# Optimization experiments

Hardware: AMD Instinct MI355X
Metric: run time of the kernel (lower is better)

The kernel has to match this reference:

```python
import jax, jax.numpy as jnp
import numpy as np

TAU = 2.0       # LIF membrane time constant (spikingjelly default)
ALPHA = 2.0     # ATan surrogate sharpness
EPS = 1e-5      # BN eps
NUM_HEADS = 12
PATCH = 2
LENTH = 256     # (H/PATCH)*(W/PATCH)

@jax.custom_vjp
def heaviside(x):
    return (x >= 0.0).astype(x.dtype)

def _hv_fwd(x):
    return heaviside(x), x

def _hv_bwd(x, g):
    sg = ALPHA / 2.0 / (1.0 + (jnp.pi / 2.0 * ALPHA * x) ** 2)  # ATan surrogate
    return (g * sg,)

heaviside.defvjp(_hv_fwd, _hv_bwd)

def lif(x):
    # multi-step LIF over leading time axis, hard reset, v_th = 1.0
    def step(v, xt):
        v = v + (xt - v) / TAU
        s = heaviside(v - 1.0)
        return v * (1.0 - s), s
    _, s = jax.lax.scan(step, jnp.zeros_like(x[0]), x)
    return s

def setup_inputs() -> dict:
    key = jax.random.key(0)
    ks = jax.random.split(key, 9)
    T, B, C, H, W = 4, 4, 384, 32, 32
    x = jax.random.normal(ks[0], (T, B, C, H, W), dtype=jnp.float32)
    Wconv = jax.random.normal(ks[1], (2 * C, C, PATCH, PATCH), dtype=jnp.float32) * (1.0 / np.sqrt(C * PATCH * PATCH))
    gamma1 = jax.random.uniform(ks[2], (2 * C,), dtype=jnp.float32, minval=0.5, maxval=1.5)
    beta1 = jax.random.normal(ks[3], (2 * C,), dtype=jnp.float32) * 0.1
    Wproj = jax.random.normal(ks[4], (C, C), dtype=jnp.float32) * (1.0 / np.sqrt(C))
    gamma2 = jax.random.uniform(ks[5], (C,), dtype=jnp.float32, minval=0.5, maxval=1.5)
    beta2 = jax.random.normal(ks[6], (C,), dtype=jnp.float32) * 0.1
    firing_rate_x = jax.random.uniform(ks[7], (1, 1, NUM_HEADS, 1, 1), dtype=jnp.float32, minval=0.05, maxval=0.5)
    firing_rate_attn = jax.random.uniform(ks[8], (1, 1, NUM_HEADS, 1, 1), dtype=jnp.float32, minval=0.05, maxval=0.5)
    return {"x": x, "Wconv": Wconv, "gamma1": gamma1, "beta1": beta1, "Wproj": Wproj,
            "gamma2": gamma2, "beta2": beta2, "firing_rate_x": firing_rate_x,
            "firing_rate_attn": firing_rate_attn}

def reference(x, Wconv, gamma1, beta1, Wproj, gamma2, beta2, firing_rate_x, firing_rate_attn):
    T, B, C, H, W = x.shape
    d = C // NUM_HEADS
    xs = lif(x)                                          # spikes [T,B,C,H,W]
    # patch conv dim -> 2*dim, stride = kernel = PATCH (eval BN: running mean 0, var 1)
    y = jax.lax.conv_general_dilated(xs.reshape(T * B, C, H, W), Wconv,
                                     (PATCH, PATCH), 'VALID',
                                     dimension_numbers=('NCHW', 'OIHW', 'NCHW'))
    bn1 = gamma1 / jnp.sqrt(1.0 + EPS)
    y = y * bn1[None, :, None, None] + beta1[None, :, None, None]
    Np = (H // PATCH) * (W // PATCH)                     # == LENTH
    y = y.reshape(T, B, NUM_HEADS, 2 * d, Np)
    y1, y2 = y[:, :, :, :d, :], y[:, :, :, d:, :]
    xr = xs.reshape(T, B, NUM_HEADS, d, H * W)
    scale1 = 1.0 / jnp.sqrt(firing_rate_x * d)
    attn = jnp.einsum('tbhdn,tbhdm->tbhnm', y1, xr) * scale1   # [T,B,h,Np,HW]
    attn = lif(attn)
    scale2 = 1.0 / jnp.sqrt(firing_rate_attn * LENTH)
    out = jnp.einsum('tbhdn,tbhnm->tbhdm', y2, attn) * scale2  # [T,B,h,d,HW]
    out = out.reshape(T, B, C, H, W)
    out = lif(out)
    out = jnp.einsum('oc,tbchw->tbohw', Wproj, out)            # 1x1 conv proj
    bn2 = gamma2 / jnp.sqrt(1.0 + EPS)
    out = out * bn2[None, None, :, None, None] + beta2[None, None, :, None, None]
    return out + x
```

## Files before the change

### kernel.cpp

```cpp
#include <hip/hip_runtime.h>
#include <hip/hip_bf16.h>
#include <math.h>


typedef __attribute__((ext_vector_type(8))) short short8;
typedef __attribute__((ext_vector_type(4))) float f32x4;

#define T_ 4
#define B_ 4
#define C_ 384
#define HW 1024
#define NH_ 12
#define Np_ 256
#define EPS_ 1e-5f
#define LDK 56

static __device__ __forceinline__ unsigned short f2bf(float f) {
    __hip_bfloat16 h = __float2bfloat16(f);
    return *reinterpret_cast<unsigned short*>(&h);
}
static __device__ __forceinline__ float bf2f(unsigned short u) {
    __hip_bfloat16 h = *reinterpret_cast<__hip_bfloat16*>(&u);
    return __bfloat162float(h);
}
static __device__ __forceinline__ void split3(float w, unsigned short& u0,
                                              unsigned short& u1, unsigned short& u2) {
    u0 = f2bf(w);  float f0 = bf2f(u0);
    float r1 = w - f0;
    u1 = f2bf(r1); float f1 = bf2f(u1);
    u2 = f2bf(r1 - f1);
}

__global__ __launch_bounds__(256) void k_wsplit(const float* __restrict__ Wc,
                                                const float* __restrict__ Wp,
                                                unsigned short* __restrict__ Wc3,
                                                unsigned short* __restrict__ Wp3) {
    const int NC = 768 * 1536;
    const int NP = 384 * 384;
    int i = blockIdx.x * 256 + threadIdx.x;
    float w; unsigned short* dst; int idx, plane;
    if (i < NC) { w = Wc[i]; dst = Wc3; idx = i; plane = NC; }
    else {
        int j = i - NC;
        if (j >= NP) return;
        w = Wp[j]; dst = Wp3; idx = j; plane = NP;
    }
    unsigned short u0, u1, u2;
    split3(w, u0, u1, u2);
    dst[idx] = u0; dst[plane + idx] = u1; dst[2 * plane + idx] = u2;
}

__global__ __launch_bounds__(256) void k_lif_im2col(const float* __restrict__ x,
                                                    unsigned short* __restrict__ Bc,
                                                    unsigned short* __restrict__ xsb) {
    int gt = blockIdx.x * 256 + threadIdx.x;
    int pw = gt & 15, ph = (gt >> 4) & 15;
    int v = gt >> 8;
    int c = v % 384, b = v / 384;
    float v00 = 0.f, v01 = 0.f, v10 = 0.f, v11 = 0.f;
    const size_t xrow = ((size_t)b * C_ + c) * HW + (size_t)(2 * ph) * 32 + 2 * pw;
#pragma unroll
    for (int t = 0; t < T_; ++t) {
        const float* px = x + (size_t)t * (B_ * C_ * HW) + xrow;
        float2 r0 = *(const float2*)px;
        float2 r1 = *(const float2*)(px + 32);
        v00 += (r0.x - v00) * 0.5f;
        v01 += (r0.y - v01) * 0.5f;
        v10 += (r1.x - v10) * 0.5f;
        v11 += (r1.y - v11) * 0.5f;
        ushort4 s;
        s.x = (v00 >= 1.f) ? 0x3F80 : 0; if (v00 >= 1.f) v00 = 0.f;
        s.y = (v01 >= 1.f) ? 0x3F80 : 0; if (v01 >= 1.f) v01 = 0.f;
        s.z = (v10 >= 1.f) ? 0x3F80 : 0; if (v10 >= 1.f) v10 = 0.f;
        s.w = (v11 >= 1.f) ? 0x3F80 : 0; if (v11 >= 1.f) v11 = 0.f;
        int tb = t * B_ + b;
        int n = tb * 256 + ph * 16 + pw;
        *(ushort4*)(Bc + (size_t)n * 1536 + 4 * c) = s;
        size_t xo = ((size_t)tb * C_ + c) * HW + (size_t)(2 * ph) * 32 + 2 * pw;
        ushort2 w0 = {s.x, s.y}, w1 = {s.z, s.w};
        *(ushort2*)(xsb + xo) = w0;
        *(ushort2*)(xsb + xo + 32) = w1;
    }
}

__global__ __launch_bounds__(256) void k_mconv(const unsigned short* __restrict__ Bc,
                                               const unsigned short* __restrict__ Wc3,
                                               const float* __restrict__ g1,
                                               const float* __restrict__ b1,
                                               const float* __restrict__ frx,
                                               const float* __restrict__ fra,
                                               unsigned short* __restrict__ y1s,
                                               unsigned short* __restrict__ y2s) {
    __shared__ short As[3][48][LDK];
    __shared__ short Bs[128][LDK];
    const int nb = blockIdx.x, mb = blockIdx.y;
    const int tid = threadIdx.x;
    const int lane = tid & 63, wv = tid >> 6;
    const int quad = lane >> 4, lr = lane & 15;
    f32x4 acc[3][2];
#pragma unroll
    for (int mi = 0; mi < 3; ++mi)
#pragma unroll
        for (int in = 0; in < 2; ++in)
            acc[mi][in] = (f32x4){0.f, 0.f, 0.f, 0.f};

    const int arow = tid >> 2, akoff = (tid & 3) * 8;
    for (int k0 = 0; k0 < 1536; k0 += 32) {
        if (tid < 192) {
#pragma unroll
            for (int s = 0; s < 3; ++s) {
                short8 a = *(const short8*)(Wc3 + ((size_t)(s * 768 + mb * 48 + arow)) * 1536 + k0 + akoff);
                *(short8*)&As[s][arow][akoff] = a;
            }
        }
#pragma unroll
        for (int i = 0; i < 2; ++i) {
            int f = i * 256 + tid;
            int row = f >> 2, koff = (f & 3) * 8;
            short8 bv = *(const short8*)(Bc + ((size_t)(nb * 128 + row)) * 1536 + k0 + koff);
            *(short8*)&Bs[row][koff] = bv;
        }
        __syncthreads();
        short8 bf[2], af[3][3];
#pragma unroll
        for (int in = 0; in < 2; ++in)
            bf[in] = *(const short8*)&Bs[wv * 32 + in * 16 + lr][quad * 8];
#pragma unroll
        for (int s = 0; s < 3; ++s)
#pragma unroll
            for (int mi = 0; mi < 3; ++mi)
                af[s][mi] = *(const short8*)&As[s][mi * 16 + lr][quad * 8];
#pragma unroll
        for (int s = 0; s < 3; ++s)
#pragma unroll
            for (int mi = 0; mi < 3; ++mi)
#pragma unroll
                for (int in = 0; in < 2; ++in)
                    acc[mi][in] = __builtin_amdgcn_mfma_f32_16x16x32_bf16(af[s][mi], bf[in], acc[mi][in], 0, 0, 0);
        __syncthreads();
    }
    const float rs = 1.0f / sqrtf(1.0f + EPS_);
#pragma unroll
    for (int mi = 0; mi < 3; ++mi) {
        const int g16 = 3 * mb + mi;
        const int h = g16 >> 2;
        const int rr16 = (g16 & 3) * 16;
        const bool isy1 = (rr16 < 32);
        const float scl = isy1 ? (1.0f / sqrtf(frx[h] * 32.0f))
                               : (1.0f / sqrtf(fra[h] * 256.0f));
#pragma unroll
        for (int in = 0; in < 2; ++in) {
            int n_g = nb * 128 + wv * 32 + in * 16 + lr;
            int tb = n_g >> 8, pn = n_g & 255;
            size_t base = (size_t)(tb * NH_ + h) * 3 * 8192;
            ushort4 o0, o1, o2;
#pragma unroll
            for (int r = 0; r < 4; ++r) {
                int oc = h * 64 + rr16 + quad * 4 + r;
                float val = (acc[mi][in][r] * (g1[oc] * rs) + b1[oc]) * scl;
                unsigned short u0, u1, u2;
                split3(val, u0, u1, u2);
                ((unsigned short*)&o0)[r] = u0;
                ((unsigned short*)&o1)[r] = u1;
                ((unsigned short*)&o2)[r] = u2;
            }
            if (isy1) {
                int dd = rr16 + quad * 4;
                *(ushort4*)&y1s[base + 0 * 8192 + (size_t)pn * 32 + dd] = o0;
                *(ushort4*)&y1s[base + 1 * 8192 + (size_t)pn * 32 + dd] = o1;
                *(ushort4*)&y1s[base + 2 * 8192 + (size_t)pn * 32 + dd] = o2;
            } else {
                int dd = (rr16 - 32) + quad * 4;
#pragma unroll
                for (int r = 0; r < 4; ++r) {
                    y2s[base + 0 * 8192 + (size_t)(dd + r) * 256 + pn] = ((unsigned short*)&o0)[r];
                    y2s[base + 1 * 8192 + (size_t)(dd + r) * 256 + pn] = ((unsigned short*)&o1)[r];
                    y2s[base + 2 * 8192 + (size_t)(dd + r) * 256 + pn] = ((unsigned short*)&o2)[r];
                }
            }
        }
    }
}

__global__ __launch_bounds__(256, 2) void k_attn_qk(const unsigned short* __restrict__ xsb,
                                                    const unsigned short* __restrict__ y1s,
                                                    unsigned short* __restrict__ abq) {
    __shared__ unsigned short xb[4][64][40];
    const int h = blockIdx.y, b = blockIdx.z;
    const int tid = threadIdx.x;
    const int lane = tid & 63, wq = tid >> 6;
    const int quad = lane >> 4, lr = lane & 15;
    const int m0 = blockIdx.x * 64;

#pragma unroll
    for (int i = 0; i < 8; ++i) {
        int e = tid + i * 256;
        int j4 = e & 15, d = (e >> 4) & 31, t = e >> 9;
        ushort4 v = *(const ushort4*)(xsb + ((size_t)((t * B_ + b) * C_) + h * 32 + d) * HW + m0 + j4 * 4);
        xb[t][j4 * 4 + 0][d] = v.x;
        xb[t][j4 * 4 + 1][d] = v.y;
        xb[t][j4 * 4 + 2][d] = v.z;
        xb[t][j4 * 4 + 3][d] = v.w;
    }
    __syncthreads();

    float vat[4][4][4];
#pragma unroll
    for (int mi = 0; mi < 4; ++mi)
#pragma unroll
        for (int itl = 0; itl < 4; ++itl)
#pragma unroll
            for (int r = 0; r < 4; ++r) vat[mi][itl][r] = 0.f;

#pragma unroll
    for (int t = 0; t < T_; ++t) {
        const int tb = t * B_ + b;
        const size_t slab = (size_t)(tb * NH_ + h) * 3 * 8192;

        short8 af[3][4];
        const unsigned short* y1p = y1s + slab + (size_t)(wq * 64 + lr) * 32 + quad * 8;
#pragma unroll
        for (int s = 0; s < 3; ++s)
#pragma unroll
            for (int itl = 0; itl < 4; ++itl)
                af[s][itl] = *(const short8*)(y1p + s * 8192 + itl * 512);

#pragma unroll
        for (int mi = 0; mi < 4; ++mi) {
            short8 bx = *(const short8*)&xb[t][mi * 16 + lr][quad * 8];
            f32x4 acc[4];
#pragma unroll
            for (int itl = 0; itl < 4; ++itl) acc[itl] = (f32x4){0.f, 0.f, 0.f, 0.f};
#pragma unroll
            for (int s = 0; s < 3; ++s)
#pragma unroll
                for (int itl = 0; itl < 4; ++itl)
                    acc[itl] = __builtin_amdgcn_mfma_f32_16x16x32_bf16(af[s][itl], bx, acc[itl], 0, 0, 0);

            unsigned int q = 0;
#pragma unroll
            for (int itl = 0; itl < 4; ++itl)
#pragma unroll
                for (int r = 0; r < 4; ++r) {
                    float v = vat[mi][itl][r];
                    v += (acc[itl][r] - v) * 0.5f;
                    bool s = (v >= 1.0f);
                    vat[mi][itl][r] = s ? 0.f : v;
                    q |= (s ? 1u : 0u) << (itl * 4 + r);
                }
            int m = m0 + mi * 16 + lr;
            abq[(((size_t)(tb * NH_ + h) * 1024 + m) * 4 + quad) * 4 + wq] = (unsigned short)q;
        }
    }
}

__global__ __launch_bounds__(256, 1) void k_attn_pv(const unsigned long long* __restrict__ abits,
                                                    const unsigned short* __restrict__ y2s,
                                                    unsigned short* __restrict__ obt) {
    const int h = blockIdx.y, b = blockIdx.z;
    const int tid = threadIdx.x;
    const int lane = tid & 63, wv = tid >> 6;
    const int quad = lane >> 4, lr = lane & 15;
    const int dt = wv >> 1, mg = wv & 1;
    const int mbase = blockIdx.x * 64 + mg * 32;
    const int obase = (quad & 2) << 1;

    float vo[2][4];
#pragma unroll
    for (int mi = 0; mi < 2; ++mi)
#pragma unroll
        for (int r = 0; r < 4; ++r) vo[mi][r] = 0.f;

#pragma unroll
    for (int t = 0; t < T_; ++t) {
        const int tb = t * B_ + b;
        const size_t slab = (size_t)(tb * NH_ + h) * 3 * 8192;

        short8 ay[3][8];
        const unsigned short* y2p = y2s + slab + (size_t)(dt * 16 + lr) * 256 + quad * 8;
#pragma unroll
        for (int s = 0; s < 3; ++s)
#pragma unroll
            for (int kt = 0; kt < 8; ++kt)
                ay[s][kt] = *(const short8*)(y2p + s * 8192 + kt * 32);

#pragma unroll
        for (int mi = 0; mi < 2; ++mi) {
            const int m = mbase + mi * 16 + lr;
            const unsigned long long* ap = abits + ((size_t)(tb * NH_ + h) * 1024 + m) * 4 + (quad & 1) * 2;
            unsigned long long Qa = ap[0];
            unsigned long long Qb = ap[1];

            short8 bs[8];
#pragma unroll
            for (int kt = 0; kt < 8; ++kt) {
                int o = kt * 8 + obase;
                unsigned int a4 = (unsigned int)(Qa >> o) & 15u;
                unsigned int b4 = (unsigned int)(Qb >> o) & 15u;
                union { short8 v; unsigned int w[4]; } u;
                u.w[0] = ((a4 & 1u) ? 0x3F80u : 0u) | ((a4 & 2u) ? 0x3F800000u : 0u);
                u.w[1] = ((a4 & 4u) ? 0x3F80u : 0u) | ((a4 & 8u) ? 0x3F800000u : 0u);
                u.w[2] = ((b4 & 1u) ? 0x3F80u : 0u) | ((b4 & 2u) ? 0x3F800000u : 0u);
                u.w[3] = ((b4 & 4u) ? 0x3F80u : 0u) | ((b4 & 8u) ? 0x3F800000u : 0u);
                bs[kt] = u.v;
            }

            f32x4 acc2 = (f32x4){0.f, 0.f, 0.f, 0.f};
#pragma unroll
            for (int s = 0; s < 3; ++s)
#pragma unroll
                for (int kt = 0; kt < 8; ++kt)
                    acc2 = __builtin_amdgcn_mfma_f32_16x16x32_bf16(ay[s][kt], bs[kt], acc2, 0, 0, 0);

            ushort4 ob;
#pragma unroll
            for (int r = 0; r < 4; ++r) {
                float v = vo[mi][r];
                v += (acc2[r] - v) * 0.5f;
                bool s = (v >= 1.0f);
                ((unsigned short*)&ob)[r] = s ? 0x3F80 : 0;
                vo[mi][r] = s ? 0.f : v;
            }
            *(ushort4*)(obt + ((size_t)tb * HW + m) * C_ + h * 32 + dt * 16 + quad * 4) = ob;
        }
    }
}

__global__ __launch_bounds__(256) void k_mproj(const unsigned short* __restrict__ obt,
                                               const unsigned short* __restrict__ Wp3,
                                               const float* __restrict__ g2,
                                               const float* __restrict__ b2,
                                               const float* __restrict__ x,
                                               float* __restrict__ out) {
    __shared__ short As[3][64][LDK];
    __shared__ short Bs[128][LDK];
    const int nb = blockIdx.x, mb = blockIdx.y;
    const int tid = threadIdx.x;
    const int lane = tid & 63, wave = tid >> 6;
    const int wm = wave >> 1, wn = wave & 1;
    const int quad = lane >> 4, lr = lane & 15;
    const int arow = tid >> 2, akoff = (tid & 3) * 8;
    f32x4 acc[2][4];
#pragma unroll
    for (int im = 0; im < 2; ++im)
#pragma unroll
        for (int in = 0; in < 4; ++in)
            acc[im][in] = (f32x4){0.f, 0.f, 0.f, 0.f};

    for (int k0 = 0; k0 < 384; k0 += 32) {
#pragma unroll
        for (int s = 0; s < 3; ++s) {
            short8 a = *(const short8*)(Wp3 + ((size_t)(s * 384 + mb * 64 + arow)) * 384 + k0 + akoff);
            *(short8*)&As[s][arow][akoff] = a;
        }
#pragma unroll
        for (int i = 0; i < 2; ++i) {
            int f = i * 256 + tid;
            int row = f >> 2, koff = (f & 3) * 8;
            short8 bv = *(const short8*)(obt + ((size_t)(nb * 128 + row)) * 384 + k0 + koff);
            *(short8*)&Bs[row][koff] = bv;
        }
        __syncthreads();
        short8 bf[4], af[3][2];
#pragma unroll
        for (int in = 0; in < 4; ++in)
            bf[in] = *(const short8*)&Bs[wn * 64 + in * 16 + lr][quad * 8];
#pragma unroll
        for (int s = 0; s < 3; ++s)
#pragma unroll
            for (int im = 0; im < 2; ++im)
                af[s][im] = *(const short8*)&As[s][wm * 32 + im * 16 + lr][quad * 8];
#pragma unroll
        for (int s = 0; s < 3; ++s)
#pragma unroll
            for (int im = 0; im < 2; ++im)
#pragma unroll
                for (int in = 0; in < 4; ++in)
                    acc[im][in] = __builtin_amdgcn_mfma_f32_16x16x32_bf16(af[s][im], bf[in], acc[im][in], 0, 0, 0);
        __syncthreads();
    }
    const float rs = 1.0f / sqrtf(1.0f + EPS_);
#pragma unroll
    for (int im = 0; im < 2; ++im) {
#pragma unroll
        for (int in = 0; in < 4; ++in) {
            int n_g = nb * 128 + wn * 64 + in * 16 + lr;
            int tb = n_g >> 10, hw = n_g & 1023;
#pragma unroll
            for (int r = 0; r < 4; ++r) {
                int o = mb * 64 + wm * 32 + im * 16 + quad * 4 + r;
                size_t idx = ((size_t)tb * C_ + o) * HW + hw;
                out[idx] = acc[im][in][r] * (g2[o] * rs) + b2[o] + x[idx];
            }
        }
    }
}

extern "C" void kernel_launch(void* const* d_in, const int* in_sizes, int n_in,
                              void* d_out, int out_size, void* d_ws, size_t ws_size,
                              hipStream_t stream) {
    const float* x      = (const float*)d_in[0];
    const float* Wconv  = (const float*)d_in[1];
    const float* gamma1 = (const float*)d_in[2];
    const float* beta1  = (const float*)d_in[3];
    const float* Wproj  = (const float*)d_in[4];
    const float* gamma2 = (const float*)d_in[5];
    const float* beta2  = (const float*)d_in[6];
    const float* frx    = (const float*)d_in[7];
    const float* fra    = (const float*)d_in[8];
    float* out = (float*)d_out;

    unsigned short* ws16 = (unsigned short*)d_ws;
    unsigned short* Bc  = ws16;
    unsigned short* obt = ws16;
    unsigned short* Wc3 = ws16 + 6291456;
    unsigned short* Wp3 = ws16 + 9830400;
    unsigned short* xsb = ws16 + 10272768;
    unsigned short* y1s = ws16 + 16564224;
    unsigned short* y2s = ws16 + 21282816;
    unsigned long long* abits = (unsigned long long*)(ws16 + 26001408);

    k_wsplit<<<5184, 256, 0, stream>>>(Wconv, Wproj, Wc3, Wp3);
    k_lif_im2col<<<1536, 256, 0, stream>>>(x, Bc, xsb);
    k_mconv<<<dim3(32, 16), 256, 0, stream>>>(Bc, Wc3, gamma1, beta1, frx, fra, y1s, y2s);
    k_attn_qk<<<dim3(16, 12, 4), 256, 0, stream>>>(xsb, y1s, (unsigned short*)abits);
    k_attn_pv<<<dim3(16, 12, 4), 256, 0, stream>>>(abits, y2s, obt);
    k_mproj<<<dim3(128, 6), 256, 0, stream>>>(obt, Wp3, gamma2, beta2, x, out);
}
```

Before: 253.8 us.

## Use direct global-to-LDS loads in conv GEMM and shrink M tile to 32

The patch-conv GEMM now stages its A (3-way bf16 split weights) and B (im2col spikes) tiles with global_load_lds 16-byte direct-to-LDS transfers, which skip the register round trip. The LDS layout becomes unpadded 32-wide rows to match that instruction's contiguous per-wave write pattern. The M tile drops from 48 to 32 rows and the grid grows from 16 to 24 M-blocks, giving more blocks and fewer accumulators per thread. The unpadded LDS rows may cause bank conflicts on the fragment reads, and the loop still uses a single buffer with two barriers per k step.

New measurement: 254.5 us. About the same (+0.3%).

```diff
diff --git a/kernel.cpp b/kernel.cpp
--- a/kernel.cpp
+++ b/kernel.cpp
@@ -29,6 +29,12 @@
     float r1 = w - f0;
     u1 = f2bf(r1); float f1 = bf2f(u1);
     u2 = f2bf(r1 - f1);
+}
+
+typedef const __attribute__((address_space(1))) unsigned int* gas_t;
+typedef __attribute__((address_space(3))) unsigned int* las_t;
+static __device__ __forceinline__ void gl_lds16(const void* g, void* l) {
+    __builtin_amdgcn_global_load_lds((gas_t)g, (las_t)(unsigned long long)(uintptr_t)l, 16, 0, 0);
 }
 
 __global__ __launch_bounds__(256) void k_wsplit(const float* __restrict__ Wc,
@@ -91,60 +97,60 @@
                                                const float* __restrict__ fra,
                                                unsigned short* __restrict__ y1s,
                                                unsigned short* __restrict__ y2s) {
-    __shared__ short As[3][48][LDK];
-    __shared__ short Bs[128][LDK];
+    __shared__ unsigned short As[96 * 32];
+    __shared__ unsigned short Bs[128 * 32];
     const int nb = blockIdx.x, mb = blockIdx.y;
     const int tid = threadIdx.x;
     const int lane = tid & 63, wv = tid >> 6;
     const int quad = lane >> 4, lr = lane & 15;
-    f32x4 acc[3][2];
-#pragma unroll
-    for (int mi = 0; mi < 3; ++mi)
+    const int lrow = lane >> 2;
+    const int lk8 = (lane & 3) * 8;
+
+    f32x4 acc[2][2];
+#pragma unroll
+    for (int mi = 0; mi < 2; ++mi)
 #pragma unroll
         for (int in = 0; in < 2; ++in)
             acc[mi][in] = (f32x4){0.f, 0.f, 0.f, 0.f};
 
-    const int arow = tid >> 2, akoff = (tid & 3) * 8;
     for (int k0 = 0; k0 < 1536; k0 += 32) {
-        if (tid < 192) {
-#pragma unroll
-            for (int s = 0; s < 3; ++s) {
-                short8 a = *(const short8*)(Wc3 + ((size_t)(s * 768 + mb * 48 + arow)) * 1536 + k0 + akoff);
-                *(short8*)&As[s][arow][akoff] = a;
-            }
-        }
-#pragma unroll
-        for (int i = 0; i < 2; ++i) {
-            int f = i * 256 + tid;
-            int row = f >> 2, koff = (f & 3) * 8;
-            short8 bv = *(const short8*)(Bc + ((size_t)(nb * 128 + row)) * 1536 + k0 + koff);
-            *(short8*)&Bs[row][koff] = bv;
+        for (int c = wv; c < 14; c += 4) {
+            if (c < 6) {
+                int row = c * 16 + lrow;
+                const unsigned short* g = Wc3 + ((size_t)((row >> 5) * 768 + mb * 32 + (row & 31))) * 1536 + k0 + lk8;
+                gl_lds16(g, As + c * 512);
+            } else {
+                int row = (c - 6) * 16 + lrow;
+                const unsigned short* g = Bc + ((size_t)(nb * 128 + row)) * 1536 + k0 + lk8;
+                gl_lds16(g, Bs + (c - 6) * 512);
+            }
         }
         __syncthreads();
-        short8 bf[2], af[3][3];
+        short8 af[3][2], bf[2];
+#pragma unroll
+        for (int s = 0; s < 3; ++s)
+#pragma unroll
+            for (int mi = 0; mi < 2; ++mi)
+                af[s][mi] = *(const short8*)&As[(s * 32 + mi * 16 + lr) * 32 + quad * 8];
 #pragma unroll
         for (int in = 0; in < 2; ++in)
-            bf[in] = *(const short8*)&Bs[wv * 32 + in * 16 + lr][quad * 8];
-#pragma unroll
-        for (int s = 0; s < 3; ++s)
-#pragma unroll
-            for (int mi = 0; mi < 3; ++mi)
-                af[s][mi] = *(const short8*)&As[s][mi * 16 + lr][quad * 8];
-#pragma unroll
-        for (int s = 0; s < 3; ++s)
-#pragma unroll
-            for (int mi = 0; mi < 3; ++mi)
+            bf[in] = *(const short8*)&Bs[(wv * 32 + in * 16 + lr) * 32 + quad * 8];
+#pragma unroll
+        for (int s = 0; s < 3; ++s)
+#pragma unroll
+            for (int mi = 0; mi < 2; ++mi)
 #pragma unroll
                 for (int in = 0; in < 2; ++in)
                     acc[mi][in] = __builtin_amdgcn_mfma_f32_16x16x32_bf16(af[s][mi], bf[in], acc[mi][in], 0, 0, 0);
         __syncthreads();
     }
+
     const float rs = 1.0f / sqrtf(1.0f + EPS_);
 #pragma unroll
-    for (int mi = 0; mi < 3; ++mi) {
-        const int g16 = 3 * mb + mi;
-        const int h = g16 >> 2;
-        const int rr16 = (g16 & 3) * 16;
+    for (int mi = 0; mi < 2; ++mi) {
+        const int oc16 = mb * 32 + mi * 16;
+        const int h = oc16 >> 6;
+        const int rr16 = oc16 & 63;
         const bool isy1 = (rr16 < 32);
         const float scl = isy1 ? (1.0f / sqrtf(frx[h] * 32.0f))
                                : (1.0f / sqrtf(fra[h] * 256.0f));
@@ -156,7 +162,7 @@
             ushort4 o0, o1, o2;
 #pragma unroll
             for (int r = 0; r < 4; ++r) {
-                int oc = h * 64 + rr16 + quad * 4 + r;
+                int oc = oc16 + quad * 4 + r;
                 float val = (acc[mi][in][r] * (g1[oc] * rs) + b1[oc]) * scl;
                 unsigned short u0, u1, u2;
                 split3(val, u0, u1, u2);
@@ -422,7 +428,7 @@
 
     k_wsplit<<<5184, 256, 0, stream>>>(Wconv, Wproj, Wc3, Wp3);
     k_lif_im2col<<<1536, 256, 0, stream>>>(x, Bc, xsb);
-    k_mconv<<<dim3(32, 16), 256, 0, stream>>>(Bc, Wc3, gamma1, beta1, frx, fra, y1s, y2s);
+    k_mconv<<<dim3(32, 24), 256, 0, stream>>>(Bc, Wc3, gamma1, beta1, frx, fra, y1s, y2s);
     k_attn_qk<<<dim3(16, 12, 4), 256, 0, stream>>>(xsb, y1s, (unsigned short*)abits);
     k_attn_pv<<<dim3(16, 12, 4), 256, 0, stream>>>(abits, y2s, obt);
     k_mproj<<<dim3(128, 6), 256, 0, stream>>>(obt, Wp3, gamma2, beta2, x, out);
```
